# Performance work log

Measured on AMD Instinct MI355X. Metric: run time of the kernel, lower is better.

The kernel has to match this reference:

```python
import jax, jax.numpy as jnp
import numpy as np

N_WIRES = 10
DIM = 1 << N_WIRES  # 1024
EPS = 1e-12

_CNOT = jnp.array([[1, 0, 0, 0],
                   [0, 1, 0, 0],
                   [0, 0, 0, 1],
                   [0, 0, 1, 0]], dtype=jnp.complex64)

# signs[i, j] = (-1)^{bit_j(i)} for single-Z Pauli string on wire j (qubit 0 = MSB)
_bits = (np.arange(DIM)[:, None] >> (N_WIRES - 1 - np.arange(N_WIRES))[None, :]) & 1
_Z_SIGNS = jnp.asarray(1.0 - 2.0 * _bits, dtype=jnp.float32)  # (DIM, N_WIRES)


def _rx_gate(theta):
    c = jnp.cos(theta / 2).astype(jnp.complex64)
    s = jnp.sin(theta / 2).astype(jnp.complex64)
    return jnp.stack([jnp.stack([c, -1j * s]), jnp.stack([-1j * s, c])])


def _ry_gate(theta):
    c = jnp.cos(theta / 2).astype(jnp.complex64)
    s = jnp.sin(theta / 2).astype(jnp.complex64)
    return jnp.stack([jnp.stack([c, -s]), jnp.stack([s, c])])


def _apply_1q(psi, gate, q):
    # psi: (N, DIM) complex64; apply 2x2 gate on qubit q (qubit 0 = MSB)
    N = psi.shape[0]
    left, right = 1 << q, 1 << (N_WIRES - 1 - q)
    psi = psi.reshape(N, left, 2, right)
    psi = jnp.einsum('ab,nxby->nxay', gate, psi)
    return psi.reshape(N, DIM)


def _apply_2q(psi, gate, q0, q1):
    # gate: (4,4) acting on qubits (q0, q1) in that order
    G = gate.reshape(2, 2, 2, 2)
    if q0 > q1:
        G = jnp.transpose(G, (1, 0, 3, 2))
        q0, q1 = q1, q0
    N = psi.shape[0]
    a = 1 << q0
    b = 1 << (q1 - q0 - 1)
    c = 1 << (N_WIRES - 1 - q1)
    psi = psi.reshape(N, a, 2, b, 2, c)
    psi = jnp.einsum('ijkl,nxkylz->nxiyjz', G, psi)
    return psi.reshape(N, DIM)


def setup_inputs() -> dict:
    key = jax.random.key(0)
    k1, k2, k3, k4 = jax.random.split(key, 4)
    x = jax.random.normal(k1, (4, 1024, DIM), dtype=jnp.float32)
    rx0 = jax.random.normal(k2, (N_WIRES,), dtype=jnp.float32)
    ry0 = jax.random.normal(k3, (N_WIRES,), dtype=jnp.float32)
    ry1 = jax.random.normal(k4, (N_WIRES,), dtype=jnp.float32)
    return {"x": x, "rx0": rx0, "ry0": ry0, "ry1": ry1}


def reference(x, rx0, ry0, ry1):
    B, T, C = x.shape
    x_flat = x.reshape(B * T, C)
    # amplitude encoding: L2-normalize each row into a complex state vector
    norm = jnp.linalg.norm(x_flat, axis=1, keepdims=True)
    psi = (x_flat / jnp.maximum(norm, EPS)).astype(jnp.complex64)  # (N, DIM)
    # layer 1: RX then RY on each wire
    for j in range(N_WIRES):
        psi = _apply_1q(psi, _rx_gate(rx0[j]), j)
        psi = _apply_1q(psi, _ry_gate(ry0[j]), j)
    # CNOT ring
    for j in range(N_WIRES):
        psi = _apply_2q(psi, _CNOT, j, (j + 1) % N_WIRES)
    # layer 2: RY on each wire
    for j in range(N_WIRES):
        psi = _apply_1q(psi, _ry_gate(ry1[j]), j)
    # expectation values of Z on each wire: sum_i |psi_i|^2 * (-1)^{bit_j(i)}
    probs = psi.real ** 2 + psi.imag ** 2  # (N, DIM) float32
    out = probs @ _Z_SIGNS                  # (N, N_WIRES)
    return out.reshape(B, T, N_WIRES).astype(jnp.float32)
```

## Files before the change

kernel.cpp:

```cpp
#include <hip/hip_runtime.h>

#define NW 10
typedef float f32x2 __attribute__((ext_vector_type(2)));

__device__ __forceinline__ f32x2 pk_mul(f32x2 a, f32x2 b) {
    f32x2 d;
    asm("v_pk_mul_f32 %0, %1, %2" : "=v"(d) : "v"(a), "v"(b));
    return d;
}
__device__ __forceinline__ f32x2 pk_fma(f32x2 a, f32x2 b, f32x2 c) {
    f32x2 d;
    asm("v_pk_fma_f32 %0, %1, %2, %3" : "=v"(d) : "v"(a), "v"(b), "v"(c));
    return d;
}
__device__ __forceinline__ f32x2 pk_fma_sw1(f32x2 a, f32x2 b, f32x2 c) {
    f32x2 d;
    asm("v_pk_fma_f32 %0, %1, %2, %3 op_sel:[0,1,0] op_sel_hi:[1,0,1]"
        : "=v"(d) : "v"(a), "v"(b), "v"(c));
    return d;
}
__device__ __forceinline__ f32x2 sp2(float x)           { return f32x2{ x,  x}; }
__device__ __forceinline__ f32x2 sp2pm(float x)         { return f32x2{ x, -x}; }
__device__ __forceinline__ f32x2 sp2mp(float x)         { return f32x2{-x,  x}; }

__device__ __forceinline__ int gperm(int v) {
    #pragma unroll
    for (int k = 9; k >= 0; --k) {
        const int cs = 9 - k;
        const int ts = 9 - ((k + 1) % NW);
        v ^= ((v >> cs) & 1) << ts;
    }
    return v;
}

__device__ __forceinline__ int PF(int i) {
    return i + ((i >> 5) << 2) + ((i >> 8) << 3);
}
#define PBUF 1176

__device__ __forceinline__ float rl(float v, int lane) {
    return __int_as_float(__builtin_amdgcn_readlane(__float_as_int(v), lane));
}

template<int D>
__device__ __forceinline__ void cgv(f32x2* rf, f32x2* mf,
                                    float ar, float ai, float br, float bi) {
    const f32x2 sAr = sp2(ar),  sAi  = sp2(ai),  sAiN = sp2(-ai);
    const f32x2 sBr = sp2(br),  sBrN = sp2(-br);
    const f32x2 sBi = sp2(bi),  sBiN = sp2(-bi);
    #pragma unroll
    for (int base = 0; base < 8; base += 2 * D) {
        #pragma unroll
        for (int off = 0; off < D; ++off) {
            const int j0 = base + off, j1 = j0 + D;
            const f32x2 v0r = rf[j0], v0i = mf[j0];
            const f32x2 v1r = rf[j1], v1i = mf[j1];
            f32x2 t = pk_mul(sAr, v0r);
            t = pk_fma(sAiN, v0i, t); t = pk_fma(sBr, v1r, t);
            rf[j0] = pk_fma(sBiN, v1i, t);
            t = pk_mul(sAr, v0i);
            t = pk_fma(sAi, v0r, t);  t = pk_fma(sBr, v1i, t);
            mf[j0] = pk_fma(sBi, v1r, t);
            t = pk_mul(sAr, v1r);
            t = pk_fma(sAi, v1i, t);  t = pk_fma(sBrN, v0r, t);
            rf[j1] = pk_fma(sBiN, v0i, t);
            t = pk_mul(sAr, v1i);
            t = pk_fma(sAiN, v1r, t); t = pk_fma(sBrN, v0i, t);
            mf[j1] = pk_fma(sBi, v0r, t);
        }
    }
}

__device__ __forceinline__ void cgv0(f32x2* rf, f32x2* mf,
                                     float ar, float ai, float br, float bi) {
    const f32x2 sAr  = sp2(ar);
    const f32x2 sAiN = sp2mp(ai);
    const f32x2 sAiP = sp2pm(ai);
    const f32x2 sBrN = sp2pm(br);
    const f32x2 sBiN = sp2(-bi);
    const f32x2 sBi  = sp2(bi);
    #pragma unroll
    for (int j = 0; j < 8; ++j) {
        const f32x2 vr = rf[j], vi = mf[j];
        f32x2 t = pk_mul(sAr, vr);
        t = pk_fma(sAiN, vi, t);
        t = pk_fma_sw1(sBrN, vr, t);
        rf[j] = pk_fma_sw1(sBiN, vi, t);
        t = pk_mul(sAr, vi);
        t = pk_fma(sAiP, vr, t);
        t = pk_fma_sw1(sBrN, vi, t);
        mf[j] = pk_fma_sw1(sBi, vr, t);
    }
}

template<int D>
__device__ __forceinline__ void rgv(f32x2* rf, f32x2* mf, float c, float s) {
    const f32x2 sC = sp2(c), sS = sp2(s), sSN = sp2(-s);
    #pragma unroll
    for (int base = 0; base < 8; base += 2 * D) {
        #pragma unroll
        for (int off = 0; off < D; ++off) {
            const int j0 = base + off, j1 = j0 + D;
            const f32x2 v0r = rf[j0], v0i = mf[j0];
            const f32x2 v1r = rf[j1], v1i = mf[j1];
            rf[j0] = pk_fma(sSN, v1r, pk_mul(sC, v0r));
            mf[j0] = pk_fma(sSN, v1i, pk_mul(sC, v0i));
            rf[j1] = pk_fma(sC, v1r, pk_mul(sS, v0r));
            mf[j1] = pk_fma(sC, v1i, pk_mul(sS, v0i));
        }
    }
}

__device__ __forceinline__ void rgv0(f32x2* rf, f32x2* mf, float c, float s) {
    const f32x2 sC = sp2(c), sSN = sp2mp(s);
    #pragma unroll
    for (int j = 0; j < 8; ++j) {
        const f32x2 vr = rf[j], vi = mf[j];
        rf[j] = pk_fma_sw1(sSN, vr, pk_mul(sC, vr));
        mf[j] = pk_fma_sw1(sSN, vi, pk_mul(sC, vi));
    }
}

__global__ __launch_bounds__(64) void qsa_main(
    const float* __restrict__ x,
    const float* __restrict__ rx0,
    const float* __restrict__ ry0,
    const float* __restrict__ ry1,
    float* __restrict__ out) {

    __shared__ __align__(16) float reb[PBUF];
    __shared__ __align__(16) float imb[PBUF];

    const int t = threadIdx.x;
    const int n = blockIdx.x;

    f32x2 rf[8], mf[8];
    const float* xr = x + ((size_t)n << 10) + (t << 4);
    #pragma unroll
    for (int k = 0; k < 4; ++k) {
        const float4 v = *reinterpret_cast<const float4*>(xr + 4 * k);
        rf[2*k]   = f32x2{v.x, v.y};
        rf[2*k+1] = f32x2{v.z, v.w};
    }

    float car = 0.f, cai = 0.f, cbr = 0.f, cbi = 0.f, cc1 = 0.f, cs1 = 0.f;
    if (t < NW) {
        float sx, cx, sy0, cy0;
        sincosf(0.5f * rx0[t], &sx,  &cx);
        sincosf(0.5f * ry0[t], &sy0, &cy0);
        sincosf(0.5f * ry1[t], &cs1, &cc1);
        car =  cy0 * cx;  cai =  sy0 * sx;
        cbr = -sy0 * cx;  cbi = -cy0 * sx;
    }

    f32x2 ssv = {0.f, 0.f};
    #pragma unroll
    for (int j = 0; j < 8; ++j) ssv += rf[j] * rf[j];
    float ss = ssv.x + ssv.y;
    #pragma unroll
    for (int b = 32; b > 0; b >>= 1) ss += __shfl_xor(ss, b, 64);
    const float scale = 1.0f / fmaxf(sqrtf(ss), 1e-12f);

    {
        const float ar = rl(car,9), ai = rl(cai,9), br = rl(cbr,9), bi = rl(cbi,9);
        const f32x2 sSc  = sp2(scale);
        const f32x2 sAr  = sp2(ar);
        const f32x2 sAiP = sp2pm(ai);
        const f32x2 sBrN = sp2pm(br);
        const f32x2 sBi  = sp2(bi);
        #pragma unroll
        for (int j = 0; j < 8; ++j) {
            const f32x2 v = pk_mul(sSc, rf[j]);
            rf[j] = pk_fma_sw1(sBrN, v, pk_mul(sAr, v));
            mf[j] = pk_fma_sw1(sBi,  v, pk_mul(sAiP, v));
        }
    }
    cgv<1>(rf, mf, rl(car,8), rl(cai,8), rl(cbr,8), rl(cbi,8));
    cgv<2>(rf, mf, rl(car,7), rl(cai,7), rl(cbr,7), rl(cbi,7));
    cgv<4>(rf, mf, rl(car,6), rl(cai,6), rl(cbr,6), rl(cbi,6));

    #pragma unroll
    for (int k = 0; k < 4; ++k) {
        const int p = PF((t << 4) + 4 * k);
        *reinterpret_cast<float4*>(&reb[p]) =
            make_float4(rf[2*k].x, rf[2*k].y, rf[2*k+1].x, rf[2*k+1].y);
        *reinterpret_cast<float4*>(&imb[p]) =
            make_float4(mf[2*k].x, mf[2*k].y, mf[2*k+1].x, mf[2*k+1].y);
    }
    __syncthreads();
    {
        const int b0 = ((t >> 4) << 8) | (t & 15);
        #pragma unroll
        for (int j = 0; j < 8; ++j) {
            const int p0 = PF(b0 + ((2*j) << 4)), p1 = PF(b0 + ((2*j+1) << 4));
            rf[j] = f32x2{reb[p0], reb[p1]};
            mf[j] = f32x2{imb[p0], imb[p1]};
        }
    }

    cgv0  (rf, mf, rl(car,5), rl(cai,5), rl(cbr,5), rl(cbi,5));
    cgv<1>(rf, mf, rl(car,4), rl(cai,4), rl(cbr,4), rl(cbi,4));
    cgv<2>(rf, mf, rl(car,3), rl(cai,3), rl(cbr,3), rl(cbi,3));
    cgv<4>(rf, mf, rl(car,2), rl(cai,2), rl(cbr,2), rl(cbi,2));

    __syncthreads();
    {
        const int b0 = ((t >> 4) << 8) | (t & 15);
        #pragma unroll
        for (int j = 0; j < 8; ++j) {
            const int p0 = PF(b0 + ((2*j) << 4)), p1 = PF(b0 + ((2*j+1) << 4));
            reb[p0] = rf[j].x; reb[p1] = rf[j].y;
            imb[p0] = mf[j].x; imb[p1] = mf[j].y;
        }
    }
    __syncthreads();
    #pragma unroll
    for (int k = 0; k < 4; ++k) {
        const int p = PF((k << 8) | (t << 2));
        const float4 qr = *reinterpret_cast<const float4*>(&reb[p]);
        const float4 qi = *reinterpret_cast<const float4*>(&imb[p]);
        rf[2*k] = f32x2{qr.x, qr.y}; rf[2*k+1] = f32x2{qr.z, qr.w};
        mf[2*k] = f32x2{qi.x, qi.y}; mf[2*k+1] = f32x2{qi.z, qi.w};
    }

    cgv<2>(rf, mf, rl(car,1), rl(cai,1), rl(cbr,1), rl(cbi,1));
    cgv<4>(rf, mf, rl(car,0), rl(cai,0), rl(cbr,0), rl(cbi,0));

    __syncthreads();
    #pragma unroll
    for (int k = 0; k < 4; ++k) {
        const int p = PF((k << 8) | (t << 2));
        *reinterpret_cast<float4*>(&reb[p]) =
            make_float4(rf[2*k].x, rf[2*k].y, rf[2*k+1].x, rf[2*k+1].y);
        *reinterpret_cast<float4*>(&imb[p]) =
            make_float4(mf[2*k].x, mf[2*k].y, mf[2*k+1].x, mf[2*k+1].y);
    }
    __syncthreads();
    {
        const int gt = gperm(t << 4);
        #pragma unroll
        for (int j = 0; j < 8; ++j) {
            const int p0 = PF(gt ^ gperm(2*j)), p1 = PF(gt ^ gperm(2*j+1));
            rf[j] = f32x2{reb[p0], reb[p1]};
            mf[j] = f32x2{imb[p0], imb[p1]};
        }
    }

    rgv0  (rf, mf, rl(cc1,9), rl(cs1,9));
    rgv<1>(rf, mf, rl(cc1,8), rl(cs1,8));
    rgv<2>(rf, mf, rl(cc1,7), rl(cs1,7));
    rgv<4>(rf, mf, rl(cc1,6), rl(cs1,6));

    __syncthreads();
    #pragma unroll
    for (int k = 0; k < 4; ++k) {
        const int p = PF((t << 4) + 4 * k);
        *reinterpret_cast<float4*>(&reb[p]) =
            make_float4(rf[2*k].x, rf[2*k].y, rf[2*k+1].x, rf[2*k+1].y);
        *reinterpret_cast<float4*>(&imb[p]) =
            make_float4(mf[2*k].x, mf[2*k].y, mf[2*k+1].x, mf[2*k+1].y);
    }
    __syncthreads();
    {
        const int b0 = ((t >> 4) << 8) | (t & 15);
        #pragma unroll
        for (int j = 0; j < 8; ++j) {
            const int p0 = PF(b0 + ((2*j) << 4)), p1 = PF(b0 + ((2*j+1) << 4));
            rf[j] = f32x2{reb[p0], reb[p1]};
            mf[j] = f32x2{imb[p0], imb[p1]};
        }
    }

    rgv0  (rf, mf, rl(cc1,5), rl(cs1,5));
    rgv<1>(rf, mf, rl(cc1,4), rl(cs1,4));
    rgv<2>(rf, mf, rl(cc1,3), rl(cs1,3));
    rgv<4>(rf, mf, rl(cc1,2), rl(cs1,2));

    __syncthreads();
    {
        const int b0 = ((t >> 4) << 8) | (t & 15);
        #pragma unroll
        for (int j = 0; j < 8; ++j) {
            const int p0 = PF(b0 + ((2*j) << 4)), p1 = PF(b0 + ((2*j+1) << 4));
            reb[p0] = rf[j].x; reb[p1] = rf[j].y;
            imb[p0] = mf[j].x; imb[p1] = mf[j].y;
        }
    }
    __syncthreads();
    #pragma unroll
    for (int k = 0; k < 4; ++k) {
        const int p = PF((k << 8) | (t << 2));
        const float4 qr = *reinterpret_cast<const float4*>(&reb[p]);
        const float4 qi = *reinterpret_cast<const float4*>(&imb[p]);
        rf[2*k] = f32x2{qr.x, qr.y}; rf[2*k+1] = f32x2{qr.z, qr.w};
        mf[2*k] = f32x2{qi.x, qi.y}; mf[2*k+1] = f32x2{qi.z, qi.w};
    }

    rgv<2>(rf, mf, rl(cc1,1), rl(cs1,1));
    rgv<4>(rf, mf, rl(cc1,0), rl(cs1,0));

    f32x2 accP = {0,0}, acc9 = {0,0}, acc8 = {0,0}, acc1 = {0,0}, acc0 = {0,0};
    const f32x2 pm = {1.f, -1.f};
    #pragma unroll
    for (int j = 0; j < 8; ++j) {
        const f32x2 p = rf[j]*rf[j] + mf[j]*mf[j];
        accP += p;
        acc9 += pm * p;
        if (j & 1) acc8 -= p; else acc8 += p;
        if (j & 2) acc1 -= p; else acc1 += p;
        if (j & 4) acc0 -= p; else acc0 += p;
    }
    float P  = accP.x + accP.y;
    float a9 = acc9.x + acc9.y;
    float a8 = acc8.x + acc8.y;
    float a1 = acc1.x + acc1.y;
    float a0 = acc0.x + acc0.y;
    #pragma unroll
    for (int b = 1; b < 64; b <<= 1) {
        a0 += __shfl_xor(a0, b, 64);
        a1 += __shfl_xor(a1, b, 64);
        a8 += __shfl_xor(a8, b, 64);
        a9 += __shfl_xor(a9, b, 64);
        const float e = __shfl_xor(P, b, 64);
        P = (t & b) ? (e - P) : (e + P);
    }
    float* o = out + (size_t)n * NW;
    if (t == 0) { o[0] = a0; o[1] = a1; o[8] = a8; o[9] = a9; }
    if (t == 32) o[2] = P;
    if (t == 16) o[3] = P;
    if (t ==  8) o[4] = P;
    if (t ==  4) o[5] = P;
    if (t ==  2) o[6] = P;
    if (t ==  1) o[7] = P;
}

extern "C" void kernel_launch(void* const* d_in, const int* in_sizes, int n_in,
                              void* d_out, int out_size, void* d_ws, size_t ws_size,
                              hipStream_t stream) {
    const float* x   = (const float*)d_in[0];
    const float* rx0 = (const float*)d_in[1];
    const float* ry0 = (const float*)d_in[2];
    const float* ry1 = (const float*)d_in[3];
    float* out = (float*)d_out;
    const int nstates = in_sizes[0] >> 10;
    qsa_main<<<nstates, 64, 0, stream>>>(x, rx0, ry0, ry1, out);
}
```

Measured before the change: 82.87 us.

## Apply low-lane qubit gates via DPP lane swaps to cut LDS transposes

Measured after the change: 81.55 us. No clear change (-1.6%).

```diff
diff --git a/kernel.cpp b/kernel.cpp
--- a/kernel.cpp
+++ b/kernel.cpp
@@ -19,9 +19,17 @@
         : "=v"(d) : "v"(a), "v"(b), "v"(c));
     return d;
 }
-__device__ __forceinline__ f32x2 sp2(float x)           { return f32x2{ x,  x}; }
-__device__ __forceinline__ f32x2 sp2pm(float x)         { return f32x2{ x, -x}; }
-__device__ __forceinline__ f32x2 sp2mp(float x)         { return f32x2{-x,  x}; }
+__device__ __forceinline__ f32x2 sp2(float x)   { return f32x2{ x,  x}; }
+__device__ __forceinline__ f32x2 sp2pm(float x) { return f32x2{ x, -x}; }
+__device__ __forceinline__ f32x2 sp2mp(float x) { return f32x2{-x,  x}; }
+
+template<int CTRL>
+__device__ __forceinline__ f32x2 dpp2(f32x2 v) {
+    f32x2 d;
+    d.x = __int_as_float(__builtin_amdgcn_mov_dpp(__float_as_int(v.x), CTRL, 0xF, 0xF, true));
+    d.y = __int_as_float(__builtin_amdgcn_mov_dpp(__float_as_int(v.y), CTRL, 0xF, 0xF, true));
+    return d;
+}
 
 __device__ __forceinline__ int gperm(int v) {
     #pragma unroll
@@ -93,6 +101,30 @@
     }
 }
 
+template<int CTRL>
+__device__ __forceinline__ void cgd(f32x2* rf, f32x2* mf, float sg,
+                                    float ar, float ai, float br, float bi) {
+    const f32x2 sAr   = sp2(ar);
+    const f32x2 sAiS  = sp2(sg * ai);
+    const f32x2 sAiSN = sp2(-sg * ai);
+    const f32x2 sBrS  = sp2(sg * br);
+    const f32x2 sBi   = sp2(bi);
+    const f32x2 sBiN  = sp2(-bi);
+    #pragma unroll
+    for (int j = 0; j < 8; ++j) {
+        const f32x2 orr = rf[j], oii = mf[j];
+        const f32x2 prr = dpp2<CTRL>(orr), pii = dpp2<CTRL>(oii);
+        f32x2 t = pk_mul(sAr, orr);
+        t = pk_fma(sAiSN, oii, t);
+        t = pk_fma(sBrS, prr, t);
+        rf[j] = pk_fma(sBiN, pii, t);
+        t = pk_mul(sAr, oii);
+        t = pk_fma(sAiS, orr, t);
+        t = pk_fma(sBrS, pii, t);
+        mf[j] = pk_fma(sBi, prr, t);
+    }
+}
+
 template<int D>
 __device__ __forceinline__ void rgv(f32x2* rf, f32x2* mf, float c, float s) {
     const f32x2 sC = sp2(c), sS = sp2(s), sSN = sp2(-s);
@@ -121,6 +153,16 @@
     }
 }
 
+template<int CTRL>
+__device__ __forceinline__ void rgd(f32x2* rf, f32x2* mf, float sg, float c, float s) {
+    const f32x2 sC = sp2(c), sS = sp2(-sg * s);
+    #pragma unroll
+    for (int j = 0; j < 8; ++j) {
+        rf[j] = pk_fma(sS, dpp2<CTRL>(rf[j]), pk_mul(sC, rf[j]));
+        mf[j] = pk_fma(sS, dpp2<CTRL>(mf[j]), pk_mul(sC, mf[j]));
+    }
+}
+
 __global__ __launch_bounds__(64) void qsa_main(
     const float* __restrict__ x,
     const float* __restrict__ rx0,
@@ -160,6 +202,9 @@
     #pragma unroll
     for (int b = 32; b > 0; b >>= 1) ss += __shfl_xor(ss, b, 64);
     const float scale = 1.0f / fmaxf(sqrtf(ss), 1e-12f);
+
+    const float sg1 = (t & 1) ? -1.f : 1.f;
+    const float sg2 = (t & 2) ? -1.f : 1.f;
 
     {
         const float ar = rl(car,9), ai = rl(cai,9), br = rl(cbr,9), bi = rl(cbi,9);
@@ -178,6 +223,8 @@
     cgv<1>(rf, mf, rl(car,8), rl(cai,8), rl(cbr,8), rl(cbi,8));
     cgv<2>(rf, mf, rl(car,7), rl(cai,7), rl(cbr,7), rl(cbi,7));
     cgv<4>(rf, mf, rl(car,6), rl(cai,6), rl(cbr,6), rl(cbi,6));
+    cgd<0xB1>(rf, mf, sg1, rl(car,5), rl(cai,5), rl(cbr,5), rl(cbi,5));
+    cgd<0x4E>(rf, mf, sg2, rl(car,4), rl(cai,4), rl(cbr,4), rl(cbi,4));
 
     #pragma unroll
     for (int k = 0; k < 4; ++k) {
@@ -188,118 +235,68 @@
             make_float4(mf[2*k].x, mf[2*k].y, mf[2*k+1].x, mf[2*k+1].y);
     }
     __syncthreads();
+    const int b1 = ((t & 3) << 4) | (t >> 2);
+    #pragma unroll
+    for (int j = 0; j < 8; ++j) {
+        const int p0 = PF(((2*j) << 6) | b1), p1 = PF(((2*j+1) << 6) | b1);
+        rf[j] = f32x2{reb[p0], reb[p1]};
+        mf[j] = f32x2{imb[p0], imb[p1]};
+    }
+
+    cgv0  (rf, mf, rl(car,3), rl(cai,3), rl(cbr,3), rl(cbi,3));
+    cgv<1>(rf, mf, rl(car,2), rl(cai,2), rl(cbr,2), rl(cbi,2));
+    cgv<2>(rf, mf, rl(car,1), rl(cai,1), rl(cbr,1), rl(cbi,1));
+    cgv<4>(rf, mf, rl(car,0), rl(cai,0), rl(cbr,0), rl(cbi,0));
+
+    __syncthreads();
+    #pragma unroll
+    for (int j = 0; j < 8; ++j) {
+        const int p0 = PF(((2*j) << 6) | b1), p1 = PF(((2*j+1) << 6) | b1);
+        reb[p0] = rf[j].x; reb[p1] = rf[j].y;
+        imb[p0] = mf[j].x; imb[p1] = mf[j].y;
+    }
+    __syncthreads();
     {
-        const int b0 = ((t >> 4) << 8) | (t & 15);
+        const int gb = gperm(b1);
         #pragma unroll
         for (int j = 0; j < 8; ++j) {
-            const int p0 = PF(b0 + ((2*j) << 4)), p1 = PF(b0 + ((2*j+1) << 4));
+            const int p0 = PF(gperm((2*j) << 6) ^ gb);
+            const int p1 = PF(gperm((2*j+1) << 6) ^ gb);
             rf[j] = f32x2{reb[p0], reb[p1]};
             mf[j] = f32x2{imb[p0], imb[p1]};
         }
     }
 
-    cgv0  (rf, mf, rl(car,5), rl(cai,5), rl(cbr,5), rl(cbi,5));
-    cgv<1>(rf, mf, rl(car,4), rl(cai,4), rl(cbr,4), rl(cbi,4));
-    cgv<2>(rf, mf, rl(car,3), rl(cai,3), rl(cbr,3), rl(cbi,3));
-    cgv<4>(rf, mf, rl(car,2), rl(cai,2), rl(cbr,2), rl(cbi,2));
-
-    __syncthreads();
-    {
-        const int b0 = ((t >> 4) << 8) | (t & 15);
-        #pragma unroll
-        for (int j = 0; j < 8; ++j) {
-            const int p0 = PF(b0 + ((2*j) << 4)), p1 = PF(b0 + ((2*j+1) << 4));
-            reb[p0] = rf[j].x; reb[p1] = rf[j].y;
-            imb[p0] = mf[j].x; imb[p1] = mf[j].y;
-        }
+    rgv<4>(rf, mf, rl(cc1,0), rl(cs1,0));
+    rgv<2>(rf, mf, rl(cc1,1), rl(cs1,1));
+    rgv<1>(rf, mf, rl(cc1,2), rl(cs1,2));
+    rgv0  (rf, mf, rl(cc1,3), rl(cs1,3));
+    rgd<0x4E>(rf, mf, sg2, rl(cc1,4), rl(cs1,4));
+    rgd<0xB1>(rf, mf, sg1, rl(cc1,5), rl(cs1,5));
+
+    __syncthreads();
+    #pragma unroll
+    for (int j = 0; j < 8; ++j) {
+        const int p0 = PF(((2*j) << 6) | b1), p1 = PF(((2*j+1) << 6) | b1);
+        reb[p0] = rf[j].x; reb[p1] = rf[j].y;
+        imb[p0] = mf[j].x; imb[p1] = mf[j].y;
     }
     __syncthreads();
     #pragma unroll
     for (int k = 0; k < 4; ++k) {
-        const int p = PF((k << 8) | (t << 2));
+        const int p = PF((t << 4) + 4 * k);
         const float4 qr = *reinterpret_cast<const float4*>(&reb[p]);
         const float4 qi = *reinterpret_cast<const float4*>(&imb[p]);
         rf[2*k] = f32x2{qr.x, qr.y}; rf[2*k+1] = f32x2{qr.z, qr.w};
         mf[2*k] = f32x2{qi.x, qi.y}; mf[2*k+1] = f32x2{qi.z, qi.w};
     }
 
-    cgv<2>(rf, mf, rl(car,1), rl(cai,1), rl(cbr,1), rl(cbi,1));
-    cgv<4>(rf, mf, rl(car,0), rl(cai,0), rl(cbr,0), rl(cbi,0));
-
-    __syncthreads();
-    #pragma unroll
-    for (int k = 0; k < 4; ++k) {
-        const int p = PF((k << 8) | (t << 2));
-        *reinterpret_cast<float4*>(&reb[p]) =
-            make_float4(rf[2*k].x, rf[2*k].y, rf[2*k+1].x, rf[2*k+1].y);
-        *reinterpret_cast<float4*>(&imb[p]) =
-            make_float4(mf[2*k].x, mf[2*k].y, mf[2*k+1].x, mf[2*k+1].y);
-    }
-    __syncthreads();
-    {
-        const int gt = gperm(t << 4);
-        #pragma unroll
-        for (int j = 0; j < 8; ++j) {
-            const int p0 = PF(gt ^ gperm(2*j)), p1 = PF(gt ^ gperm(2*j+1));
-            rf[j] = f32x2{reb[p0], reb[p1]};
-            mf[j] = f32x2{imb[p0], imb[p1]};
-        }
-    }
-
+    rgv<4>(rf, mf, rl(cc1,6), rl(cs1,6));
+    rgv<2>(rf, mf, rl(cc1,7), rl(cs1,7));
+    rgv<1>(rf, mf, rl(cc1,8), rl(cs1,8));
     rgv0  (rf, mf, rl(cc1,9), rl(cs1,9));
-    rgv<1>(rf, mf, rl(cc1,8), rl(cs1,8));
-    rgv<2>(rf, mf, rl(cc1,7), rl(cs1,7));
-    rgv<4>(rf, mf, rl(cc1,6), rl(cs1,6));
-
-    __syncthreads();
-    #pragma unroll
-    for (int k = 0; k < 4; ++k) {
-        const int p = PF((t << 4) + 4 * k);
-        *reinterpret_cast<float4*>(&reb[p]) =
-            make_float4(rf[2*k].x, rf[2*k].y, rf[2*k+1].x, rf[2*k+1].y);
-        *reinterpret_cast<float4*>(&imb[p]) =
-            make_float4(mf[2*k].x, mf[2*k].y, mf[2*k+1].x, mf[2*k+1].y);
-    }
-    __syncthreads();
-    {
-        const int b0 = ((t >> 4) << 8) | (t & 15);
-        #pragma unroll
-        for (int j = 0; j < 8; ++j) {
-            const int p0 = PF(b0 + ((2*j) << 4)), p1 = PF(b0 + ((2*j+1) << 4));
-            rf[j] = f32x2{reb[p0], reb[p1]};
-            mf[j] = f32x2{imb[p0], imb[p1]};
-        }
-    }
-
-    rgv0  (rf, mf, rl(cc1,5), rl(cs1,5));
-    rgv<1>(rf, mf, rl(cc1,4), rl(cs1,4));
-    rgv<2>(rf, mf, rl(cc1,3), rl(cs1,3));
-    rgv<4>(rf, mf, rl(cc1,2), rl(cs1,2));
-
-    __syncthreads();
-    {
-        const int b0 = ((t >> 4) << 8) | (t & 15);
-        #pragma unroll
-        for (int j = 0; j < 8; ++j) {
-            const int p0 = PF(b0 + ((2*j) << 4)), p1 = PF(b0 + ((2*j+1) << 4));
-            reb[p0] = rf[j].x; reb[p1] = rf[j].y;
-            imb[p0] = mf[j].x; imb[p1] = mf[j].y;
-        }
-    }
-    __syncthreads();
-    #pragma unroll
-    for (int k = 0; k < 4; ++k) {
-        const int p = PF((k << 8) | (t << 2));
-        const float4 qr = *reinterpret_cast<const float4*>(&reb[p]);
-        const float4 qi = *reinterpret_cast<const float4*>(&imb[p]);
-        rf[2*k] = f32x2{qr.x, qr.y}; rf[2*k+1] = f32x2{qr.z, qr.w};
-        mf[2*k] = f32x2{qi.x, qi.y}; mf[2*k+1] = f32x2{qi.z, qi.w};
-    }
-
-    rgv<2>(rf, mf, rl(cc1,1), rl(cs1,1));
-    rgv<4>(rf, mf, rl(cc1,0), rl(cs1,0));
-
-    f32x2 accP = {0,0}, acc9 = {0,0}, acc8 = {0,0}, acc1 = {0,0}, acc0 = {0,0};
+
+    f32x2 accP = {0,0}, acc9 = {0,0}, acc8 = {0,0}, acc7 = {0,0}, acc6 = {0,0};
     const f32x2 pm = {1.f, -1.f};
     #pragma unroll
     for (int j = 0; j < 8; ++j) {
@@ -307,31 +304,31 @@
         accP += p;
         acc9 += pm * p;
         if (j & 1) acc8 -= p; else acc8 += p;
-        if (j & 2) acc1 -= p; else acc1 += p;
-        if (j & 4) acc0 -= p; else acc0 += p;
+        if (j & 2) acc7 -= p; else acc7 += p;
+        if (j & 4) acc6 -= p; else acc6 += p;
     }
     float P  = accP.x + accP.y;
     float a9 = acc9.x + acc9.y;
     float a8 = acc8.x + acc8.y;
-    float a1 = acc1.x + acc1.y;
-    float a0 = acc0.x + acc0.y;
+    float a7 = acc7.x + acc7.y;
+    float a6 = acc6.x + acc6.y;
     #pragma unroll
     for (int b = 1; b < 64; b <<= 1) {
-        a0 += __shfl_xor(a0, b, 64);
-        a1 += __shfl_xor(a1, b, 64);
+        a6 += __shfl_xor(a6, b, 64);
+        a7 += __shfl_xor(a7, b, 64);
         a8 += __shfl_xor(a8, b, 64);
         a9 += __shfl_xor(a9, b, 64);
         const float e = __shfl_xor(P, b, 64);
         P = (t & b) ? (e - P) : (e + P);
     }
     float* o = out + (size_t)n * NW;
-    if (t == 0) { o[0] = a0; o[1] = a1; o[8] = a8; o[9] = a9; }
-    if (t == 32) o[2] = P;
-    if (t == 16) o[3] = P;
-    if (t ==  8) o[4] = P;
-    if (t ==  4) o[5] = P;
-    if (t ==  2) o[6] = P;
-    if (t ==  1) o[7] = P;
+    if (t == 0) { o[6] = a6; o[7] = a7; o[8] = a8; o[9] = a9; }
+    if (t ==  1) o[5] = P;
+    if (t ==  2) o[4] = P;
+    if (t ==  4) o[3] = P;
+    if (t ==  8) o[2] = P;
+    if (t == 16) o[1] = P;
+    if (t == 32) o[0] = P;
 }
 
 extern "C" void kernel_launch(void* const* d_in, const int* in_sizes, int n_in,
```
